# Kernel tuning notes

Hardware: AMD Instinct MI355X
Metric: run time of the kernel (lower is better)

The kernel has to match this reference:

```python
import jax, jax.numpy as jnp
import numpy as np

# db4 analysis filters (pywt convention); synthesis reuses same filters (orthogonal wavelet,
# correlation analysis + convolution synthesis gives perfect reconstruction under periodization).
DEC_LO = [-0.010597401784997278, 0.032883011666982945, 0.030841381835986965, -0.18703481171888114,
          -0.02798376941698385, 0.6308807679295904, 0.7148465705525415, 0.23037781330885523]
DEC_HI = [-0.23037781330885523, 0.7148465705525415, -0.6308807679295904, -0.02798376941698385,
          0.18703481171888114, 0.030841381835986965, -0.032883011666982945, -0.010597401784997278]
LEVELS = 3

def _analysis(x, filt):
    # a[n] = sum_k filt[k] * x[(2n+k) mod L]  (circular filter + downsample-by-2)
    y = sum(c * jnp.roll(x, -k, axis=-1) for k, c in enumerate(filt))
    return y[..., ::2]

def _synthesis(a, filt):
    # upsample-by-2 (zeros at odd positions) then circular convolution with filt
    u = jnp.zeros(a.shape[:-1] + (2 * a.shape[-1],), a.dtype).at[..., ::2].set(a)
    return sum(c * jnp.roll(u, k, axis=-1) for k, c in enumerate(filt))

def _decompose(z, levels):
    details, cur = [], z
    for _ in range(levels):
        details.append(_analysis(cur, DEC_HI))
        cur = _analysis(cur, DEC_LO)
    return cur, details

def _reconstruct(approx, details):
    cur = approx
    for d in reversed(details):
        cur = _synthesis(cur, DEC_LO) + _synthesis(d, DEC_HI)
    return cur

def _soft_threshold(c, lam_raw):
    # dynamic per-(batch,channel) threshold scaled by learnable softplus(lam_raw)
    lam = jax.nn.softplus(lam_raw) * jnp.mean(jnp.abs(c), axis=-1)  # [B,H]
    thr = jnp.sign(c) * jnp.maximum(jnp.abs(c) - lam[..., None], 0.0)
    return thr, lam

def _film(c, flow_raw, Wgb, bgb, Wg, bg):
    # FiLM gamma/beta from flow features, sigmoid-gated
    gb = flow_raw @ Wgb.T + bgb                      # [B, 2H]
    H = c.shape[1]
    gamma, beta = gb[:, :H], gb[:, H:]
    gate = jax.nn.sigmoid(flow_raw @ Wg + bg)[:, None, None]  # [B,1,1]
    return c * (1.0 + gate * gamma[:, :, None]) + gate * beta[:, :, None]

def setup_inputs() -> dict:
    key = jax.random.key(0)
    ks = jax.random.split(key, 8)
    B, L, C, Hd = 16, 4096, 64, 128
    x = jax.random.normal(ks[0], (B, L, C), jnp.float32)
    mask = jnp.ones((B, L), jnp.float32)
    flow_raw = jax.random.normal(ks[1], (B, 24), jnp.float32)
    W_in = jax.random.normal(ks[2], (Hd, C), jnp.float32) / np.sqrt(C)
    b_in = jnp.zeros((Hd,), jnp.float32)
    W_mix = jax.random.normal(ks[3], (Hd, Hd), jnp.float32) / np.sqrt(Hd)
    b_mix = jnp.zeros((Hd,), jnp.float32)
    lam_raw = jnp.full((LEVELS + 1,), 0.5413248538970947, jnp.float32)  # softplus^-1(1.0)
    film_Wgb = jax.random.normal(ks[4], (LEVELS + 1, 2 * Hd, 24), jnp.float32) * 0.05
    film_bgb = jnp.zeros((LEVELS + 1, 2 * Hd), jnp.float32)
    film_Wg = jax.random.normal(ks[5], (LEVELS + 1, 24), jnp.float32) * 0.05
    film_bg = jnp.zeros((LEVELS + 1,), jnp.float32)
    return dict(x=x, mask=mask, flow_raw=flow_raw, W_in=W_in, b_in=b_in, W_mix=W_mix, b_mix=b_mix,
                lam_raw=lam_raw, film_Wgb=film_Wgb, film_bgb=film_bgb, film_Wg=film_Wg, film_bg=film_bg)

def reference(x, mask, flow_raw, W_in, b_in, W_mix, b_mix, lam_raw, film_Wgb, film_bgb, film_Wg, film_bg):
    xp = x.transpose(0, 2, 1) * mask[:, None, :]               # [B,C,L]
    z = jnp.einsum('hc,bcl->bhl', W_in, xp) + b_in[:, None]    # input_proj (1x1 conv)
    approx, details = _decompose(z, LEVELS)
    approx = _film(approx, flow_raw, film_Wgb[0], film_bgb[0], film_Wg[0], film_bg[0])
    details = [_film(d, flow_raw, film_Wgb[i + 1], film_bgb[i + 1], film_Wg[i + 1], film_bg[i + 1])
               for i, d in enumerate(details)]
    approx_t, lam_a = _soft_threshold(approx, lam_raw[0])
    dts, lams = [], [lam_a]
    for i, d in enumerate(details):
        dt, lam_d = _soft_threshold(d, lam_raw[i + 1])
        dts.append(dt)
        lams.append(lam_d)
    z_rec = _reconstruct(approx_t, dts)
    mixed = jnp.einsum('gh,bhl->bgl', W_mix, z + z_rec) + b_mix[:, None]  # mix (1x1 conv)
    out = jax.nn.gelu(mixed, approximate=False)                 # torch nn.GELU is exact
    h_seq = out.transpose(0, 2, 1) * mask[..., None]            # [B,L,H]
    denom = jnp.clip(jnp.sum(mask, axis=1, keepdims=True), 1.0, None)
    h_pool = jnp.sum(h_seq * mask[..., None], axis=1) / denom   # masked mean pool [B,H]
    lam_cat = jnp.concatenate([l.reshape(l.shape[0], -1) for l in lams], axis=1)
    return h_seq, h_pool, jnp.mean(lam_cat, axis=1), jnp.max(lam_cat, axis=1)
```

## Files before the change

kernel.cpp:

```cpp
#include <hip/hip_runtime.h>
#include <math.h>

#define BB 16
#define LL 4096
#define CC 64
#define HD 128

typedef __attribute__((ext_vector_type(8))) short short8;
typedef __attribute__((ext_vector_type(8))) unsigned short ushort8;
typedef __attribute__((ext_vector_type(4))) float floatx4;

__constant__ float c_lo[8] = {
    -0.010597401784997278f, 0.032883011666982945f, 0.030841381835986965f,
    -0.18703481171888114f, -0.02798376941698385f, 0.6308807679295904f,
    0.7148465705525415f, 0.23037781330885523f};
__constant__ float c_hi[8] = {
    -0.23037781330885523f, 0.7148465705525415f, -0.6308807679295904f,
    -0.02798376941698385f, 0.18703481171888114f, 0.030841381835986965f,
    -0.032883011666982945f, -0.010597401784997278f};

__device__ __forceinline__ float gelu_fast(float x) {
    float u = x * fmaf(0.044715f * x, x, 1.0f) * 1.5957691216057308f;
    return x / (1.0f + __expf(-u));
}
__device__ __forceinline__ unsigned short f2b(float f) {
    unsigned int u = __float_as_uint(f);
    u = u + 0x7FFFu + ((u >> 16) & 1u);
    return (unsigned short)(u >> 16);
}
__device__ __forceinline__ float b2f(unsigned short s) {
    return __uint_as_float(((unsigned int)s) << 16);
}


__global__ __launch_bounds__(256) void zproj_kernel(
    const float* __restrict__ x, const float* __restrict__ mask,
    const float* __restrict__ W_in, const float* __restrict__ b_in,
    unsigned short* __restrict__ z_bf,
    const float* __restrict__ W_mix, unsigned short* __restrict__ Bmix,
    const float* __restrict__ flow, const float* __restrict__ Wgb,
    const float* __restrict__ bgb, const float* __restrict__ Wg,
    const float* __restrict__ bg, float* __restrict__ film_ws,
    float* __restrict__ gate_ws) {
    int blk = blockIdx.x;
    int tid = threadIdx.x;

    if (blk >= BB * 64) {
        int e = blk - BB * 64;
        if (e < 64) {
            int q = e * 256 + tid;
            int g = (q >> 3) & 127;
            int h = ((q >> 10) << 3) | (q & 7);
            Bmix[q] = f2b(W_mix[g * HD + h]);
        } else {
            int bf = e - 64;
            int f = bf & 3;
            int b = bf >> 2;
            const float* fl = flow + b * 24;
            const float* wrow = Wgb + ((size_t)(f * 256 + tid)) * 24;
            float acc = bgb[f * 256 + tid];
#pragma unroll
            for (int j = 0; j < 24; ++j) acc = fmaf(wrow[j], fl[j], acc);
            film_ws[(size_t)bf * 256 + tid] = acc;
            if (tid == 0) {
                float g = bg[f];
#pragma unroll
                for (int j = 0; j < 24; ++j) g = fmaf(Wg[f * 24 + j], fl[j], g);
                gate_ws[bf] = 1.0f / (1.0f + expf(-g));
            }
        }
        return;
    }

    int b = blk >> 6;
    int l0 = (blk & 63) << 6;
    int lane = tid & 63;
    int w = tid >> 6;
    int h_half = w >> 1;
    int l_q = w & 1;
    int ln15 = lane & 15, lq4 = lane >> 4;

    int lr0 = l0 + l_q * 32 + ln15;
    int lr1 = lr0 + 16;
    float mk0 = mask[(size_t)b * LL + lr0];
    float mk1 = mask[(size_t)b * LL + lr1];

    floatx4 acc[4][2];
#pragma unroll
    for (int i = 0; i < 4; ++i)
#pragma unroll
        for (int j = 0; j < 2; ++j) acc[i][j] = (floatx4){0.f, 0.f, 0.f, 0.f};

#pragma unroll
    for (int ks = 0; ks < 2; ++ks) {
        int c0 = ks * 32 + (lq4 << 3);
        short8 bf0, bf1;
        {
            const float* xp = x + ((size_t)b * LL + lr0) * CC + c0;
            float4 xa = *(const float4*)xp;
            float4 xb = *(const float4*)(xp + 4);
            bf0[0] = (short)f2b(xa.x * mk0); bf0[1] = (short)f2b(xa.y * mk0);
            bf0[2] = (short)f2b(xa.z * mk0); bf0[3] = (short)f2b(xa.w * mk0);
            bf0[4] = (short)f2b(xb.x * mk0); bf0[5] = (short)f2b(xb.y * mk0);
            bf0[6] = (short)f2b(xb.z * mk0); bf0[7] = (short)f2b(xb.w * mk0);
        }
        {
            const float* xp = x + ((size_t)b * LL + lr1) * CC + c0;
            float4 xa = *(const float4*)xp;
            float4 xb = *(const float4*)(xp + 4);
            bf1[0] = (short)f2b(xa.x * mk1); bf1[1] = (short)f2b(xa.y * mk1);
            bf1[2] = (short)f2b(xa.z * mk1); bf1[3] = (short)f2b(xa.w * mk1);
            bf1[4] = (short)f2b(xb.x * mk1); bf1[5] = (short)f2b(xb.y * mk1);
            bf1[6] = (short)f2b(xb.z * mk1); bf1[7] = (short)f2b(xb.w * mk1);
        }
        const float* wb = W_in + (size_t)(h_half * 64 + ln15) * CC + c0;
#pragma unroll
        for (int ht = 0; ht < 4; ++ht) {
            const float* wr = wb + (size_t)ht * 16 * CC;
            float4 wa = *(const float4*)wr;
            float4 wc = *(const float4*)(wr + 4);
            short8 af;
            af[0] = (short)f2b(wa.x); af[1] = (short)f2b(wa.y);
            af[2] = (short)f2b(wa.z); af[3] = (short)f2b(wa.w);
            af[4] = (short)f2b(wc.x); af[5] = (short)f2b(wc.y);
            af[6] = (short)f2b(wc.z); af[7] = (short)f2b(wc.w);
            acc[ht][0] = __builtin_amdgcn_mfma_f32_16x16x32_bf16(bf0, af, acc[ht][0], 0, 0, 0);
            acc[ht][1] = __builtin_amdgcn_mfma_f32_16x16x32_bf16(bf1, af, acc[ht][1], 0, 0, 0);
        }
    }

#pragma unroll
    for (int ht = 0; ht < 4; ++ht) {
        int h = h_half * 64 + ht * 16 + ln15;
        float bi = b_in[h];
        unsigned short* zr = z_bf + ((size_t)(b * HD + h)) * LL;
#pragma unroll
        for (int j = 0; j < 2; ++j) {
            int lbase = l0 + l_q * 32 + j * 16 + (lq4 << 2);
            ushort4 o;
            o.x = f2b(acc[ht][j][0] + bi);
            o.y = f2b(acc[ht][j][1] + bi);
            o.z = f2b(acc[ht][j][2] + bi);
            o.w = f2b(acc[ht][j][3] + bi);
            *(ushort4*)(zr + lbase) = o;
        }
    }
}


__device__ __forceinline__ void analysis_step(const float* __restrict__ src,
                                              float* __restrict__ lo_dst,
                                              float* __restrict__ hi_dst,
                                              int half, int tid) {
    int len = half << 1;
    for (int q = tid; q < (half >> 2); q += 256) {
        int n0 = q << 2;
        float lo[4], hi[4];
        if (n0 + 4 == half) {
#pragma unroll
            for (int i = 0; i < 4; ++i) {
                float l = 0.f, hh = 0.f;
#pragma unroll
                for (int k = 0; k < 8; ++k) {
                    float v = src[(2 * (n0 + i) + k) & (len - 1)];
                    l = fmaf(c_lo[k], v, l);
                    hh = fmaf(c_hi[k], v, hh);
                }
                lo[i] = l; hi[i] = hh;
            }
        } else {
            float sv[16];
            const float* sp = src + (n0 << 1);
            *(float4*)&sv[0]  = *(const float4*)(sp);
            *(float4*)&sv[4]  = *(const float4*)(sp + 4);
            *(float4*)&sv[8]  = *(const float4*)(sp + 8);
            *(float4*)&sv[12] = *(const float4*)(sp + 12);
#pragma unroll
            for (int i = 0; i < 4; ++i) {
                float l = 0.f, hh = 0.f;
#pragma unroll
                for (int k = 0; k < 8; ++k) {
                    l = fmaf(c_lo[k], sv[2 * i + k], l);
                    hh = fmaf(c_hi[k], sv[2 * i + k], hh);
                }
                lo[i] = l; hi[i] = hh;
            }
        }
        *(float4*)&lo_dst[n0] = make_float4(lo[0], lo[1], lo[2], lo[3]);
        *(float4*)&hi_dst[n0] = make_float4(hi[0], hi[1], hi[2], hi[3]);
    }
}

__device__ __forceinline__ void synth_oct(const float* __restrict__ A,
                                          const float* __restrict__ D,
                                          int m0, int half, float* ov) {
    if (m0 == 0) {
        int mask2 = (half << 1) - 1;
#pragma unroll
        for (int t = 0; t < 8; ++t) {
            int par = t & 1;
            float s = 0.f;
#pragma unroll
            for (int j = 0; j < 4; ++j) {
                int k = 2 * j + par;
                int idx = ((t - k) & mask2) >> 1;
                s = fmaf(c_lo[k], A[idx], s);
                s = fmaf(c_hi[k], D[idx], s);
            }
            ov[t] = s;
        }
    } else {
        float av[8], dv[8];
        *(float4*)&av[0] = *(const float4*)(A + m0 - 4);
        *(float4*)&av[4] = *(const float4*)(A + m0);
        *(float4*)&dv[0] = *(const float4*)(D + m0 - 4);
        *(float4*)&dv[4] = *(const float4*)(D + m0);
#pragma unroll
        for (int t = 0; t < 4; ++t) {
            float e = 0.f, o = 0.f;
#pragma unroll
            for (int j = 0; j < 4; ++j) {
                float xa = av[t + 4 - j], xd = dv[t + 4 - j];
                e = fmaf(c_lo[2 * j], xa, e);     e = fmaf(c_hi[2 * j], xd, e);
                o = fmaf(c_lo[2 * j + 1], xa, o); o = fmaf(c_hi[2 * j + 1], xd, o);
            }
            ov[2 * t] = e;
            ov[2 * t + 1] = o;
        }
    }
}

__device__ __forceinline__ void synth_step(const float* __restrict__ A,
                                           const float* __restrict__ D,
                                           float* __restrict__ dst,
                                           int half, int tid) {
    for (int q = tid; q < (half >> 2); q += 256) {
        int m0 = q << 2;
        int i0 = m0 << 1;
        float ov[8];
        synth_oct(A, D, m0, half, ov);
        *(float4*)&dst[i0]     = make_float4(ov[0], ov[1], ov[2], ov[3]);
        *(float4*)&dst[i0 + 4] = make_float4(ov[4], ov[5], ov[6], ov[7]);
    }
}


__global__ __launch_bounds__(256) void wavelet_kernel(const unsigned short* __restrict__ z_bf,
                                                      unsigned short* __restrict__ s_bf,
                                                      const float* __restrict__ film_ws,
                                                      const float* __restrict__ gate_ws,
                                                      const float* __restrict__ lam_raw,
                                                      float* __restrict__ lam_ws) {
    __shared__ unsigned int zpk[2048];
    __shared__ float d1[2048];
    __shared__ float d2[1024];
    __shared__ float Aq[2048];
    __shared__ float Bq[1024];

    int blk = blockIdx.x;
    int b = blk >> 7;
    int h = blk & 127;
    int tid = threadIdx.x;
    const uint4* zg4 = (const uint4*)(z_bf + ((size_t)(b * HD + h)) * LL);
    unsigned short* sg = s_bf + ((size_t)(b * HD + h)) * LL;

    for (int i = tid; i < 512; i += 256)
        ((uint4*)zpk)[i] = zg4[i];
    __syncthreads();

    for (int q = tid; q < 512; q += 256) {
        int n0 = q << 2;
        float sv[16];
        if (n0 == 2044) {
#pragma unroll
            for (int j = 0; j < 14; ++j) {
                int idx = (2 * n0 + j) & 4095;
                unsigned int wv = zpk[idx >> 1];
                sv[j] = b2f((unsigned short)((idx & 1) ? (wv >> 16) : (wv & 0xffffu)));
            }
            sv[14] = 0.f; sv[15] = 0.f;
        } else {
            uint4 wa = *(const uint4*)(zpk + n0);
            uint4 wb = *(const uint4*)(zpk + n0 + 4);
            unsigned int ww[8] = {wa.x, wa.y, wa.z, wa.w, wb.x, wb.y, wb.z, wb.w};
#pragma unroll
            for (int j = 0; j < 8; ++j) {
                sv[2 * j]     = b2f((unsigned short)(ww[j] & 0xffffu));
                sv[2 * j + 1] = b2f((unsigned short)(ww[j] >> 16));
            }
        }
        float lo[4], hi[4];
#pragma unroll
        for (int i = 0; i < 4; ++i) {
            float l = 0.f, hh = 0.f;
#pragma unroll
            for (int k = 0; k < 8; ++k) {
                l = fmaf(c_lo[k], sv[2 * i + k], l);
                hh = fmaf(c_hi[k], sv[2 * i + k], hh);
            }
            lo[i] = l; hi[i] = hh;
        }
        *(float4*)&Aq[n0] = make_float4(lo[0], lo[1], lo[2], lo[3]);
        *(float4*)&d1[n0] = make_float4(hi[0], hi[1], hi[2], hi[3]);
    }
    __syncthreads();
    analysis_step(Aq, Bq, d2, 1024, tid);
    __syncthreads();
    analysis_step(Bq, Aq, Aq + 512, 512, tid);
    __syncthreads();

    float sc0, sh0, sc1, sh1, sc2, sh2, sc3, sh3;
    {
        int base = b * 4;
#define FILM_COEF(bd, SC, SH)                                              \
        {   float ga = film_ws[((size_t)(base + bd)) * 256 + h];           \
            float be = film_ws[((size_t)(base + bd)) * 256 + 128 + h];     \
            float gt = gate_ws[base + bd];                                 \
            SC = 1.0f + gt * ga; SH = gt * be; }
        FILM_COEF(0, sc0, sh0) FILM_COEF(1, sc1, sh1)
        FILM_COEF(2, sc2, sh2) FILM_COEF(3, sc3, sh3)
#undef FILM_COEF
    }

    float* p0 = &Aq[tid << 2];
    float* p1 = &d1[tid << 2];
    float* p2 = &d1[1024 + (tid << 2)];
    float* p3 = &d2[tid << 2];
    bool lowhalf = (tid < 128);
    float scA = lowhalf ? sc0 : sc3, shA = lowhalf ? sh0 : sh3;

    float4 f0 = *(float4*)p0, f1 = *(float4*)p1, f2v = *(float4*)p2, f3 = *(float4*)p3;
#define FILMV(V, SC, SH)                                                   \
    { V.x = fmaf(V.x, SC, SH); V.y = fmaf(V.y, SC, SH);                    \
      V.z = fmaf(V.z, SC, SH); V.w = fmaf(V.w, SC, SH); }
    FILMV(f0, scA, shA) FILMV(f1, sc1, sh1) FILMV(f2v, sc1, sh1) FILMV(f3, sc2, sh2)
#undef FILMV
    float sA = fabsf(f0.x) + fabsf(f0.y) + fabsf(f0.z) + fabsf(f0.w);
    float s1 = fabsf(f1.x) + fabsf(f1.y) + fabsf(f1.z) + fabsf(f1.w)
             + fabsf(f2v.x) + fabsf(f2v.y) + fabsf(f2v.z) + fabsf(f2v.w);
    float s2 = fabsf(f3.x) + fabsf(f3.y) + fabsf(f3.z) + fabsf(f3.w);
#pragma unroll
    for (int off = 32; off > 0; off >>= 1) {
        sA += __shfl_xor(sA, off);
        s1 += __shfl_xor(s1, off);
        s2 += __shfl_xor(s2, off);
    }
    if ((tid & 63) == 0)
        ((float4*)Bq)[tid >> 6] = make_float4(lowhalf ? sA : 0.f, s1, s2,
                                              lowhalf ? 0.f : sA);
    __syncthreads();
    float4 r0 = ((const float4*)Bq)[0];
    float4 r1 = ((const float4*)Bq)[1];
    float4 r2 = ((const float4*)Bq)[2];
    float4 r3 = ((const float4*)Bq)[3];
    float lam0 = log1pf(expf(lam_raw[0])) * ((r0.x + r1.x + r2.x + r3.x) * (1.0f / 512.f));
    float lam1 = log1pf(expf(lam_raw[1])) * ((r0.y + r1.y + r2.y + r3.y) * (1.0f / 2048.f));
    float lam2 = log1pf(expf(lam_raw[2])) * ((r0.z + r1.z + r2.z + r3.z) * (1.0f / 1024.f));
    float lam3 = log1pf(expf(lam_raw[3])) * ((r0.w + r1.w + r2.w + r3.w) * (1.0f / 512.f));
    if (tid < 4) {
        float lam = (tid == 0) ? lam0 : (tid == 1) ? lam1 : (tid == 2) ? lam2 : lam3;
        lam_ws[((size_t)(b * 4 + tid)) * 128 + h] = lam;
    }
    float lamA = lowhalf ? lam0 : lam3;
#define THRV(V, LAM)                                                       \
    { float a;                                                             \
      a = fabsf(V.x) - (LAM); V.x = (a > 0.f) ? copysignf(a, V.x) : 0.f;   \
      a = fabsf(V.y) - (LAM); V.y = (a > 0.f) ? copysignf(a, V.y) : 0.f;   \
      a = fabsf(V.z) - (LAM); V.z = (a > 0.f) ? copysignf(a, V.z) : 0.f;   \
      a = fabsf(V.w) - (LAM); V.w = (a > 0.f) ? copysignf(a, V.w) : 0.f; }
    THRV(f0, lamA) THRV(f1, lam1) THRV(f2v, lam1) THRV(f3, lam2)
#undef THRV
    *(float4*)p0 = f0; *(float4*)p1 = f1; *(float4*)p2 = f2v; *(float4*)p3 = f3;
    __syncthreads();

    synth_step(Aq, Aq + 512, Bq, 512, tid);
    __syncthreads();
    synth_step(Bq, d2, Aq, 1024, tid);
    __syncthreads();
    for (int q = tid; q < 512; q += 256) {
        int m0 = q << 2;
        int i0 = m0 << 1;
        float ov[8];
        synth_oct(Aq, d1, m0, 2048, ov);
        uint4 zw = *(const uint4*)(zpk + (i0 >> 1));
        unsigned int zz[4] = {zw.x, zw.y, zw.z, zw.w};
        ushort8 o8;
#pragma unroll
        for (int t2 = 0; t2 < 4; ++t2) {
            float ze = b2f((unsigned short)(zz[t2] & 0xffffu));
            float zo = b2f((unsigned short)(zz[t2] >> 16));
            o8[2 * t2]     = f2b(ov[2 * t2] + ze);
            o8[2 * t2 + 1] = f2b(ov[2 * t2 + 1] + zo);
        }
        *(ushort8*)(sg + i0) = o8;
    }
}


union U32x4S8 { unsigned int u[4]; short8 s; };

__global__ __launch_bounds__(256) void mix_kernel(const unsigned short* __restrict__ s_bf,
                                                  const unsigned short* __restrict__ Bmix,
                                                  const float* __restrict__ b_mix,
                                                  const float* __restrict__ mask,
                                                  float* __restrict__ out,
                                                  float* __restrict__ pool_part) {
    __shared__ unsigned int T[HD * 32];
    __shared__ float pbuf[2][HD];

    int blk = blockIdx.x;
    int b = blk >> 6;
    int lt64 = blk & 63;
    int l0 = lt64 << 6;
    int tid = threadIdx.x;
    int lane = tid & 63;
    int w = tid >> 6;
    int l_half = w >> 1, g_half = w & 1;
    int ln15 = lane & 15, lq4 = lane >> 4;

    {
        const unsigned int* src = (const unsigned int*)s_bf;
#pragma unroll
        for (int r = 0; r < 4; ++r) {
            int q = (r << 8) + tid;
            int hh = q >> 3;
            int k = q & 7;
            uint4 v = *(const uint4*)(src + (size_t)(b * HD + hh) * (LL / 2) +
                                      (l0 >> 1) + (k << 2));
            int sw = hh & 31;
            unsigned int* tp = T + hh * 32;
            tp[((k << 2) + 0) ^ sw] = v.x;
            tp[((k << 2) + 1) ^ sw] = v.y;
            tp[((k << 2) + 2) ^ sw] = v.z;
            tp[((k << 2) + 3) ^ sw] = v.w;
        }
    }
    __syncthreads();

    floatx4 acc[2][4];
#pragma unroll
    for (int i = 0; i < 2; ++i)
#pragma unroll
        for (int j = 0; j < 4; ++j) acc[i][j] = (floatx4){0.f, 0.f, 0.f, 0.f};

    const unsigned short* Bb = Bmix + (g_half * 64 + ln15) * 8;

#pragma unroll 2
    for (int ks = 0; ks < 4; ++ks) {
        int koct = ks * 4 + lq4;
        short8 a[2], bb[4];
#pragma unroll
        for (int lt = 0; lt < 2; ++lt) {
            int l_loc = l_half * 32 + lt * 16 + ln15;
            int lp = l_loc >> 1;
            int odd = l_loc & 1;
            U32x4S8 cv;
#pragma unroll
            for (int qq = 0; qq < 4; ++qq) {
                int h0 = koct * 8 + 2 * qq;
                unsigned int w0 = T[h0 * 32 + (lp ^ (h0 & 31))];
                unsigned int w1 = T[(h0 + 1) * 32 + (lp ^ ((h0 + 1) & 31))];
                unsigned int e0 = odd ? (w0 >> 16) : (w0 & 0xffffu);
                unsigned int e1 = odd ? (w1 >> 16) : (w1 & 0xffffu);
                cv.u[qq] = e0 | (e1 << 16);
            }
            a[lt] = cv.s;
        }
#pragma unroll
        for (int gt = 0; gt < 4; ++gt)
            bb[gt] = *(const short8*)(Bb + (size_t)koct * 1024 + gt * 128);
#pragma unroll
        for (int lt = 0; lt < 2; ++lt)
#pragma unroll
            for (int gt = 0; gt < 4; ++gt)
                acc[lt][gt] = __builtin_amdgcn_mfma_f32_16x16x32_bf16(a[lt], bb[gt], acc[lt][gt], 0, 0, 0);
    }

    int gcol[4]; float bmv[4]; float pacc[4];
#pragma unroll
    for (int gt = 0; gt < 4; ++gt) {
        gcol[gt] = g_half * 64 + gt * 16 + ln15;
        bmv[gt] = b_mix[gcol[gt]];
        pacc[gt] = 0.f;
    }
#pragma unroll
    for (int lt = 0; lt < 2; ++lt) {
#pragma unroll
        for (int r = 0; r < 4; ++r) {
            int l = l0 + l_half * 32 + lt * 16 + (lq4 << 2) + r;
            float mkv = mask[(size_t)b * LL + l];
            float* orow = out + ((size_t)b * LL + l) * HD;
#pragma unroll
            for (int gt = 0; gt < 4; ++gt) {
                float v = gelu_fast(acc[lt][gt][r] + bmv[gt]) * mkv;
                orow[gcol[gt]] = v;
                pacc[gt] = fmaf(v, mkv, pacc[gt]);
            }
        }
    }
#pragma unroll
    for (int gt = 0; gt < 4; ++gt) {
        pacc[gt] += __shfl_xor(pacc[gt], 16);
        pacc[gt] += __shfl_xor(pacc[gt], 32);
    }
    if (lane < 16) {
#pragma unroll
        for (int gt = 0; gt < 4; ++gt)
            pbuf[l_half][g_half * 64 + gt * 16 + lane] = pacc[gt];
    }
    __syncthreads();
    if (tid < HD)
        pool_part[((size_t)(b * 64 + lt64)) * HD + tid] = pbuf[0][tid] + pbuf[1][tid];
}


__global__ void finalize_kernel(const float* __restrict__ pool_part,
                                const float* __restrict__ mask,
                                const float* __restrict__ lam_ws,
                                float* __restrict__ d_out) {
    const size_t OUT1 = (size_t)BB * LL * HD;
    const size_t OUT2 = OUT1 + (size_t)BB * HD;
    const size_t OUT3 = OUT2 + BB;
    int b = blockIdx.x, tid = threadIdx.x;
    __shared__ float rsum[256], rmax[256];
    __shared__ float dsh;

    float ms = 0.f;
    const float4* mp = (const float4*)(mask + (size_t)b * LL);
    for (int i = tid; i < LL / 4; i += 256) {
        float4 m = mp[i];
        ms += m.x + m.y + m.z + m.w;
    }
    rsum[tid] = ms; __syncthreads();
    for (int st = 128; st > 0; st >>= 1) {
        if (tid < st) rsum[tid] += rsum[tid + st];
        __syncthreads();
    }
    if (tid == 0) dsh = fmaxf(rsum[0], 1.0f);
    __syncthreads();
    float denom = dsh;

    if (tid < 128) {
        float s = 0.f;
        for (int blk = 0; blk < 64; ++blk)
            s += pool_part[((size_t)(b * 64 + blk)) * HD + tid];
        d_out[OUT1 + (size_t)b * HD + tid] = s / denom;
    }

    float v0 = lam_ws[(size_t)b * 512 + tid];
    float v1 = lam_ws[(size_t)b * 512 + 256 + tid];
    rsum[tid] = v0 + v1;
    rmax[tid] = fmaxf(v0, v1);
    __syncthreads();
    for (int st = 128; st > 0; st >>= 1) {
        if (tid < st) {
            rsum[tid] += rsum[tid + st];
            rmax[tid] = fmaxf(rmax[tid], rmax[tid + st]);
        }
        __syncthreads();
    }
    if (tid == 0) {
        d_out[OUT2 + b] = rsum[0] / 512.0f;
        d_out[OUT3 + b] = rmax[0];
    }
}


extern "C" void kernel_launch(void* const* d_in, const int* in_sizes, int n_in,
                              void* d_out, int out_size, void* d_ws, size_t ws_size,
                              hipStream_t stream) {
    (void)in_sizes; (void)n_in; (void)out_size; (void)ws_size;
    const float* x      = (const float*)d_in[0];
    const float* mask   = (const float*)d_in[1];
    const float* flow   = (const float*)d_in[2];
    const float* W_in   = (const float*)d_in[3];
    const float* b_in   = (const float*)d_in[4];
    const float* W_mix  = (const float*)d_in[5];
    const float* b_mix  = (const float*)d_in[6];
    const float* lam_raw= (const float*)d_in[7];
    const float* Wgb    = (const float*)d_in[8];
    const float* bgb    = (const float*)d_in[9];
    const float* Wg     = (const float*)d_in[10];
    const float* bg     = (const float*)d_in[11];

    unsigned short* z_bf = (unsigned short*)d_ws;
    unsigned short* s_bf = z_bf + (size_t)BB * HD * LL;
    float* film_ws   = (float*)(s_bf + (size_t)BB * HD * LL);
    float* gate_ws   = film_ws + BB * 4 * 256;
    float* lam_ws    = gate_ws + 64;
    float* pool_part = lam_ws + BB * 4 * 128;
    unsigned short* Bmix = (unsigned short*)(pool_part + BB * 64 * HD);

    float* out = (float*)d_out;

    hipLaunchKernelGGL(zproj_kernel, dim3(BB * 64 + 128), dim3(256), 0, stream,
                       x, mask, W_in, b_in, z_bf,
                       W_mix, Bmix, flow, Wgb, bgb, Wg, bg, film_ws, gate_ws);
    hipLaunchKernelGGL(wavelet_kernel, dim3(BB * HD), dim3(256), 0, stream,
                       z_bf, s_bf, film_ws, gate_ws, lam_raw, lam_ws);
    hipLaunchKernelGGL(mix_kernel, dim3(BB * (LL / 64)), dim3(256), 0, stream,
                       s_bf, Bmix, b_mix, mask, out, pool_part);
    hipLaunchKernelGGL(finalize_kernel, dim3(BB), dim3(256), 0, stream,
                       pool_part, mask, lam_ws, out);
}
```

Baseline: 69.10 us.

## Read z directly from global, transpose MFMA outputs for vector stores, split pool reduction

The wavelet kernel no longer stages z into shared memory. It reads bf16 inputs directly from global memory for both the analysis and the residual add, which drops 8 KB of LDS and a barrier but reads z twice from global or cache. The mix kernel swaps the MFMA operands so each lane holds four consecutive output channels, enabling float4 stores and float4 bias loads, and the pooling shuffle reduction changes to match. The finalize kernel splits the pool-part sum across all 256 threads using two halves.

New measurement: 66.67 us, median of 2. 1.04x faster.

```diff
diff --git a/kernel.cpp b/kernel.cpp
--- a/kernel.cpp
+++ b/kernel.cpp
@@ -251,7 +251,6 @@
                                                       const float* __restrict__ gate_ws,
                                                       const float* __restrict__ lam_raw,
                                                       float* __restrict__ lam_ws) {
-    __shared__ unsigned int zpk[2048];
     __shared__ float d1[2048];
     __shared__ float d2[1024];
     __shared__ float Aq[2048];
@@ -261,32 +260,24 @@
     int b = blk >> 7;
     int h = blk & 127;
     int tid = threadIdx.x;
-    const uint4* zg4 = (const uint4*)(z_bf + ((size_t)(b * HD + h)) * LL);
+    const unsigned short* zg = z_bf + ((size_t)(b * HD + h)) * LL;
     unsigned short* sg = s_bf + ((size_t)(b * HD + h)) * LL;
-
-    for (int i = tid; i < 512; i += 256)
-        ((uint4*)zpk)[i] = zg4[i];
-    __syncthreads();
 
     for (int q = tid; q < 512; q += 256) {
         int n0 = q << 2;
         float sv[16];
         if (n0 == 2044) {
 #pragma unroll
-            for (int j = 0; j < 14; ++j) {
-                int idx = (2 * n0 + j) & 4095;
-                unsigned int wv = zpk[idx >> 1];
-                sv[j] = b2f((unsigned short)((idx & 1) ? (wv >> 16) : (wv & 0xffffu)));
-            }
+            for (int j = 0; j < 14; ++j)
+                sv[j] = b2f(zg[(2 * n0 + j) & 4095]);
             sv[14] = 0.f; sv[15] = 0.f;
         } else {
-            uint4 wa = *(const uint4*)(zpk + n0);
-            uint4 wb = *(const uint4*)(zpk + n0 + 4);
-            unsigned int ww[8] = {wa.x, wa.y, wa.z, wa.w, wb.x, wb.y, wb.z, wb.w};
+            ushort8 va = *(const ushort8*)(zg + (n0 << 1));
+            ushort8 vb = *(const ushort8*)(zg + (n0 << 1) + 8);
 #pragma unroll
             for (int j = 0; j < 8; ++j) {
-                sv[2 * j]     = b2f((unsigned short)(ww[j] & 0xffffu));
-                sv[2 * j + 1] = b2f((unsigned short)(ww[j] >> 16));
+                sv[j]     = b2f(va[j]);
+                sv[8 + j] = b2f(vb[j]);
             }
         }
         float lo[4], hi[4];
@@ -382,16 +373,10 @@
         int i0 = m0 << 1;
         float ov[8];
         synth_oct(Aq, d1, m0, 2048, ov);
-        uint4 zw = *(const uint4*)(zpk + (i0 >> 1));
-        unsigned int zz[4] = {zw.x, zw.y, zw.z, zw.w};
+        ushort8 zin = *(const ushort8*)(zg + i0);
         ushort8 o8;
 #pragma unroll
-        for (int t2 = 0; t2 < 4; ++t2) {
-            float ze = b2f((unsigned short)(zz[t2] & 0xffffu));
-            float zo = b2f((unsigned short)(zz[t2] >> 16));
-            o8[2 * t2]     = f2b(ov[2 * t2] + ze);
-            o8[2 * t2 + 1] = f2b(ov[2 * t2 + 1] + zo);
-        }
+        for (int t = 0; t < 8; ++t) o8[t] = f2b(ov[t] + b2f(zin[t]));
         *(ushort8*)(sg + i0) = o8;
     }
 }
@@ -473,40 +458,48 @@
         for (int lt = 0; lt < 2; ++lt)
 #pragma unroll
             for (int gt = 0; gt < 4; ++gt)
-                acc[lt][gt] = __builtin_amdgcn_mfma_f32_16x16x32_bf16(a[lt], bb[gt], acc[lt][gt], 0, 0, 0);
-    }
-
-    int gcol[4]; float bmv[4]; float pacc[4];
+                acc[lt][gt] = __builtin_amdgcn_mfma_f32_16x16x32_bf16(bb[gt], a[lt], acc[lt][gt], 0, 0, 0);
+    }
+
+    float4 pacc4[4];
+#pragma unroll
+    for (int gt = 0; gt < 4; ++gt) pacc4[gt] = make_float4(0.f, 0.f, 0.f, 0.f);
+
+#pragma unroll
+    for (int lt = 0; lt < 2; ++lt) {
+        int l = l0 + l_half * 32 + lt * 16 + ln15;
+        float mkv = mask[(size_t)b * LL + l];
+        float* orow = out + ((size_t)b * LL + l) * HD;
+#pragma unroll
+        for (int gt = 0; gt < 4; ++gt) {
+            int g0q = g_half * 64 + gt * 16 + (lq4 << 2);
+            float4 bm = *(const float4*)&b_mix[g0q];
+            float4 v;
+            v.x = gelu_fast(acc[lt][gt][0] + bm.x) * mkv;
+            v.y = gelu_fast(acc[lt][gt][1] + bm.y) * mkv;
+            v.z = gelu_fast(acc[lt][gt][2] + bm.z) * mkv;
+            v.w = gelu_fast(acc[lt][gt][3] + bm.w) * mkv;
+            *(float4*)&orow[g0q] = v;
+            pacc4[gt].x = fmaf(v.x, mkv, pacc4[gt].x);
+            pacc4[gt].y = fmaf(v.y, mkv, pacc4[gt].y);
+            pacc4[gt].z = fmaf(v.z, mkv, pacc4[gt].z);
+            pacc4[gt].w = fmaf(v.w, mkv, pacc4[gt].w);
+        }
+    }
 #pragma unroll
     for (int gt = 0; gt < 4; ++gt) {
-        gcol[gt] = g_half * 64 + gt * 16 + ln15;
-        bmv[gt] = b_mix[gcol[gt]];
-        pacc[gt] = 0.f;
-    }
-#pragma unroll
-    for (int lt = 0; lt < 2; ++lt) {
-#pragma unroll
-        for (int r = 0; r < 4; ++r) {
-            int l = l0 + l_half * 32 + lt * 16 + (lq4 << 2) + r;
-            float mkv = mask[(size_t)b * LL + l];
-            float* orow = out + ((size_t)b * LL + l) * HD;
-#pragma unroll
-            for (int gt = 0; gt < 4; ++gt) {
-                float v = gelu_fast(acc[lt][gt][r] + bmv[gt]) * mkv;
-                orow[gcol[gt]] = v;
-                pacc[gt] = fmaf(v, mkv, pacc[gt]);
-            }
-        }
-    }
-#pragma unroll
-    for (int gt = 0; gt < 4; ++gt) {
-        pacc[gt] += __shfl_xor(pacc[gt], 16);
-        pacc[gt] += __shfl_xor(pacc[gt], 32);
-    }
-    if (lane < 16) {
+#pragma unroll
+        for (int off = 1; off <= 8; off <<= 1) {
+            pacc4[gt].x += __shfl_xor(pacc4[gt].x, off);
+            pacc4[gt].y += __shfl_xor(pacc4[gt].y, off);
+            pacc4[gt].z += __shfl_xor(pacc4[gt].z, off);
+            pacc4[gt].w += __shfl_xor(pacc4[gt].w, off);
+        }
+    }
+    if (ln15 == 0) {
 #pragma unroll
         for (int gt = 0; gt < 4; ++gt)
-            pbuf[l_half][g_half * 64 + gt * 16 + lane] = pacc[gt];
+            *(float4*)&pbuf[l_half][g_half * 64 + gt * 16 + (lq4 << 2)] = pacc4[gt];
     }
     __syncthreads();
     if (tid < HD)
@@ -539,12 +532,18 @@
     if (tid == 0) dsh = fmaxf(rsum[0], 1.0f);
     __syncthreads();
     float denom = dsh;
-
-    if (tid < 128) {
+    __syncthreads();
+
+    {
+        int hh = tid & 127, half = tid >> 7;
         float s = 0.f;
-        for (int blk = 0; blk < 64; ++blk)
-            s += pool_part[((size_t)(b * 64 + blk)) * HD + tid];
-        d_out[OUT1 + (size_t)b * HD + tid] = s / denom;
+        for (int blk = half * 32; blk < half * 32 + 32; ++blk)
+            s += pool_part[((size_t)(b * 64 + blk)) * HD + hh];
+        rsum[tid] = s;
+        __syncthreads();
+        if (tid < 128)
+            d_out[OUT1 + (size_t)b * HD + tid] = (rsum[tid] + rsum[tid + 128]) / denom;
+        __syncthreads();
     }
 
     float v0 = lam_ws[(size_t)b * 512 + tid];
```
